# Kernel optimization log

Measured on AMD Instinct MI355X. Metric: run time of the kernel, lower is better.

The kernel has to match this reference:

```python
import jax, jax.numpy as jnp
import numpy as np

N = 262144      # number of points
K = 16          # KNN neighbors -> fixed degree CSR
E = N * K
CLASS_DIM = 40


def setup_inputs() -> dict:
    key = jax.random.key(0)
    ks = jax.random.split(key, 12)
    x = jax.random.normal(ks[0], (N, 3), dtype=jnp.float32)
    indptr = (jnp.arange(N + 1, dtype=jnp.int32) * K)
    indices = jax.random.randint(ks[1], (E,), 0, N, dtype=jnp.int32)

    def xavier(k, fan_out, fan_in):
        bound = np.sqrt(6.0 / (fan_in + fan_out)).astype(np.float32)
        return jax.random.uniform(k, (fan_out, fan_in), dtype=jnp.float32,
                                  minval=-bound, maxval=bound)

    return {
        "x": x, "indptr": indptr, "indices": indices,
        "w1": xavier(ks[2], 64, 3),
        "w2": xavier(ks[3], 64, 64),
        "w3": xavier(ks[4], 64, 64),
        "w4": xavier(ks[5], 128, 64),
        "w5": xavier(ks[6], 1024, 192),
        "wf1": xavier(ks[7], 512, 1024),
        "wf2": xavier(ks[8], 256, 512),
        "wf3": xavier(ks[9], CLASS_DIM, 256),
    }


def reference(x, indptr, indices, w1, w2, w3, w4, w5, wf1, wf2, wf3):
    # mlp1, mlp2 (bias-free Linear + ReLU)
    h = jax.nn.relu(x @ w1.T)          # [N, 64]
    h = jax.nn.relu(h @ w2.T)          # [N, 64]

    # GraphMaxPooling: CSR neighbor max (segment-max over gathered rows)
    n = h.shape[0]
    e = indices.shape[0]
    deg = indptr[1:] - indptr[:-1]                                   # [N]
    seg = jnp.repeat(jnp.arange(n, dtype=jnp.int32), deg,
                     total_repeat_length=e)                          # [E]
    x_gm = jax.ops.segment_max(h[indices], seg, num_segments=n,
                               indices_are_sorted=True)              # [N, 64]

    # mlp3, mlp4
    h3 = jax.nn.relu(h @ w3.T)         # [N, 64]
    h4 = jax.nn.relu(h3 @ w4.T)        # [N, 128]

    # concat neighbor-pooled features with point features, mlp5
    hc = jnp.concatenate([x_gm, h4], axis=1)   # [N, 192]
    h5 = jax.nn.relu(hc @ w5.T)                # [N, 1024]

    # global max pool over points -> [1, 1024]
    g = jnp.max(h5, axis=0, keepdims=True)

    # classifier head (dropout in eval mode = identity)
    f = jax.nn.relu(g @ wf1.T)
    f = jax.nn.relu(f @ wf2.T)
    return f @ wf3.T                            # [1, class_dim]
```

## Files before the change

kernel.cpp:

```cpp
#include <hip/hip_runtime.h>
#include <hip/hip_bf16.h>
#include <stdint.h>

typedef unsigned short u16;
typedef __bf16 bf16x8 __attribute__((ext_vector_type(8)));
typedef float  f32x4  __attribute__((ext_vector_type(4)));
typedef u16    u16x8  __attribute__((ext_vector_type(8)));

__device__ __forceinline__ float bf2f(u16 u) {
    return __uint_as_float(((unsigned)u) << 16);
}
__device__ __forceinline__ u16 f2bf(float f) {
    unsigned u = __float_as_uint(f);
    u += 0x7fffu + ((u >> 16) & 1u);
    return (u16)(u >> 16);
}
__device__ __forceinline__ u16x8 maxu16(u16x8 a, u16x8 b) {
    u16x8 r;
    #pragma unroll
    for (int e = 0; e < 8; ++e) r[e] = a[e] > b[e] ? a[e] : b[e];
    return r;
}
__device__ __forceinline__ u16x8 shfl_xor16(u16x8 v, int mask) {
    union { u16x8 u; int i[4]; } a, r;
    a.u = v;
    #pragma unroll
    for (int t = 0; t < 4; ++t) r.i[t] = __shfl_xor(a.i[t], mask, 64);
    return r.u;
}

#define MFMA16(a, b, c) __builtin_amdgcn_mfma_f32_16x16x32_bf16(a, b, c, 0, 0, 0)

__device__ u16   h2g_buf[262144 * 64];
__device__ u16   gm_buf [262144 * 64];
__device__ u16   w3b[64 * 64];
__device__ u16   w4b[128 * 64];
__device__ u16   w5b[1024 * 192];
__device__ float g_buf[1024];
__device__ float f1_buf[512];
__device__ float f2_buf[256];

__global__ void k0_zero() { g_buf[threadIdx.x] = 0.f; }

__global__ void kcvt(const float* __restrict__ w3f, const float* __restrict__ w4f,
                     const float* __restrict__ w5f)
{
    int i = blockIdx.x * 256 + threadIdx.x;
    if (i < 4096)        w3b[i]         = f2bf(w3f[i]);
    else if (i < 12288)  w4b[i - 4096]  = f2bf(w4f[i - 4096]);
    else                 w5b[i - 12288] = f2bf(w5f[i - 12288]);
}

__global__ __launch_bounds__(256) void k1_mlp(
    const float* __restrict__ xf, const float* __restrict__ w1f,
    const float* __restrict__ w2f)
{
    __shared__ __align__(16) u16 sw1[64 * 4];
    __shared__ __align__(16) u16 sx [64 * 4];
    __shared__ __align__(16) u16 sw2[64 * 72];
    __shared__ __align__(16) u16 shA[64 * 72];
    __shared__ __align__(16) u16 sh2[64 * 72];

    const int tid = threadIdx.x;
    const int p0  = blockIdx.x * 64;

    for (int i = tid; i < 64 * 64; i += 256)
        sw2[(i >> 6) * 72 + (i & 63)] = f2bf(w2f[i]);
    if (tid < 192) {
        sw1[(tid / 3) * 4 + tid % 3] = f2bf(w1f[tid]);
        sx [(tid / 3) * 4 + tid % 3] = f2bf(xf[p0 * 3 + tid]);
    }
    __syncthreads();

    {
        int m = tid & 63, ng = tid >> 6;
        float x0 = bf2f(sx[m * 4]), x1 = bf2f(sx[m * 4 + 1]), x2 = bf2f(sx[m * 4 + 2]);
        #pragma unroll
        for (int j = 0; j < 16; ++j) {
            int n = ng * 16 + j;
            float s = x0 * bf2f(sw1[n * 4]) + x1 * bf2f(sw1[n * 4 + 1]) + x2 * bf2f(sw1[n * 4 + 2]);
            shA[m * 72 + n] = f2bf(fmaxf(s, 0.f));
        }
    }
    __syncthreads();

    const int lane = tid & 63, w = tid >> 6, q = lane >> 4, l15 = lane & 15;
    const int mrow = 16 * w;

    f32x4 acc2[4];
    #pragma unroll
    for (int nt = 0; nt < 4; ++nt) acc2[nt] = (f32x4){0.f, 0.f, 0.f, 0.f};
    #pragma unroll
    for (int s = 0; s < 2; ++s) {
        bf16x8 a = *(const bf16x8*)&shA[(mrow + l15) * 72 + s * 32 + q * 8];
        #pragma unroll
        for (int nt = 0; nt < 4; ++nt) {
            bf16x8 b = *(const bf16x8*)&sw2[(nt * 16 + l15) * 72 + s * 32 + q * 8];
            acc2[nt] = MFMA16(a, b, acc2[nt]);
        }
    }
    #pragma unroll
    for (int nt = 0; nt < 4; ++nt)
        #pragma unroll
        for (int r = 0; r < 4; ++r) {
            int m = mrow + q * 4 + r;
            sh2[m * 72 + nt * 16 + l15] = f2bf(fmaxf(acc2[nt][r], 0.f));
        }
    __syncthreads();

    {
        int row = tid >> 2, c = (tid & 3) * 16;
        *(u16x8*)&h2g_buf[(size_t)p0 * 64 + tid * 16]     = *(const u16x8*)&sh2[row * 72 + c];
        *(u16x8*)&h2g_buf[(size_t)p0 * 64 + tid * 16 + 8] = *(const u16x8*)&sh2[row * 72 + c + 8];
    }
}

__global__ __launch_bounds__(256) void k2_pool(const int* __restrict__ idx)
{
    const size_t p = (blockIdx.x << 2) | (threadIdx.x >> 6);
    const int lane = threadIdx.x & 63;
    const int k = lane >> 3, c = lane & 7;

    int j0 = idx[p * 16 + k];
    int j1 = idx[p * 16 + 8 + k];
    u16x8 a = *(const u16x8*)&h2g_buf[(size_t)j0 * 64 + c * 8];
    u16x8 b = *(const u16x8*)&h2g_buf[(size_t)j1 * 64 + c * 8];
    u16x8 m = maxu16(a, b);
    m = maxu16(m, shfl_xor16(m, 8));
    m = maxu16(m, shfl_xor16(m, 16));
    m = maxu16(m, shfl_xor16(m, 32));
    if (lane < 8)
        *(u16x8*)&gm_buf[p * 64 + lane * 8] = m;
}

__global__ __launch_bounds__(256) void k3_fused(int* __restrict__ g)
{
    __shared__ __align__(16) u16 lds[128 * 192 + 2 * 128 * 64];
    u16* sA  = lds;
    u16* sB0 = lds + 24576;
    u16* sB1 = lds + 24576 + 8192;

    const int tid  = threadIdx.x;
    const size_t R0 = (size_t)blockIdx.x * 128;
    const int lane = tid & 63, w = tid >> 6, q = lane >> 4, l15 = lane & 15;
    const int m0w  = (w & 1) * 64, n0w = (w >> 1) * 64;

    #pragma unroll
    for (int c = 0; c < 4; ++c) {
        int i = c * 256 + tid, r = i >> 3, js = i & 7;
        *(u16x8*)&sB0[r * 64 + ((js ^ r) & 7) * 8] =
            *(const u16x8*)&h2g_buf[(R0 + r) * 64 + js * 8];
    }
    #pragma unroll
    for (int c = 0; c < 4; ++c) {
        int i = c * 256 + tid, r = i >> 3, js = i & 7;
        *(u16x8*)&sA[r * 192 + ((js ^ r) & 7) * 8] =
            *(const u16x8*)&gm_buf[(R0 + r) * 64 + js * 8];
    }
    __syncthreads();

    {
        f32x4 a3[2][4];
        #pragma unroll
        for (int mt = 0; mt < 2; ++mt)
            #pragma unroll
            for (int nt = 0; nt < 4; ++nt) a3[mt][nt] = (f32x4){0.f, 0.f, 0.f, 0.f};
        #pragma unroll
        for (int ss = 0; ss < 2; ++ss) {
            bf16x8 a[2], b[4];
            #pragma unroll
            for (int mt = 0; mt < 2; ++mt) {
                int r = w * 32 + mt * 16 + l15;
                a[mt] = *(const bf16x8*)&sB0[r * 64 + (((ss * 4 + q) ^ r) & 7) * 8];
            }
            #pragma unroll
            for (int nt = 0; nt < 4; ++nt)
                b[nt] = *(const bf16x8*)&w3b[(nt * 16 + l15) * 64 + ss * 32 + q * 8];
            #pragma unroll
            for (int mt = 0; mt < 2; ++mt)
                #pragma unroll
                for (int nt = 0; nt < 4; ++nt)
                    a3[mt][nt] = MFMA16(a[mt], b[nt], a3[mt][nt]);
        }
        __syncthreads();
        #pragma unroll
        for (int mt = 0; mt < 2; ++mt)
            #pragma unroll
            for (int nt = 0; nt < 4; ++nt)
                #pragma unroll
                for (int r = 0; r < 4; ++r) {
                    int m = w * 32 + mt * 16 + q * 4 + r;
                    int n = nt * 16 + l15;
                    sB0[m * 64 + (((n >> 3) ^ m) & 7) * 8 + (n & 7)] =
                        f2bf(fmaxf(a3[mt][nt][r], 0.f));
                }
    }
    __syncthreads();

    {
        f32x4 a4[2][8];
        #pragma unroll
        for (int mt = 0; mt < 2; ++mt)
            #pragma unroll
            for (int nt = 0; nt < 8; ++nt) a4[mt][nt] = (f32x4){0.f, 0.f, 0.f, 0.f};
        #pragma unroll
        for (int ss = 0; ss < 2; ++ss) {
            bf16x8 a[2];
            #pragma unroll
            for (int mt = 0; mt < 2; ++mt) {
                int r = w * 32 + mt * 16 + l15;
                a[mt] = *(const bf16x8*)&sB0[r * 64 + (((ss * 4 + q) ^ r) & 7) * 8];
            }
            #pragma unroll
            for (int nt = 0; nt < 8; ++nt) {
                bf16x8 b = *(const bf16x8*)&w4b[(nt * 16 + l15) * 64 + ss * 32 + q * 8];
                #pragma unroll
                for (int mt = 0; mt < 2; ++mt)
                    a4[mt][nt] = MFMA16(a[mt], b, a4[mt][nt]);
            }
        }
        #pragma unroll
        for (int mt = 0; mt < 2; ++mt)
            #pragma unroll
            for (int nt = 0; nt < 8; ++nt)
                #pragma unroll
                for (int r = 0; r < 4; ++r) {
                    int m  = w * 32 + mt * 16 + q * 4 + r;
                    int n4 = nt * 16 + l15;
                    int j  = 8 + (n4 >> 3);
                    int p  = (j & 24) | ((j ^ m) & 7);
                    sA[m * 192 + p * 8 + (n4 & 7)] = f2bf(fmaxf(a4[mt][nt][r], 0.f));
                }
    }
    __syncthreads();

    u16x8 v[4];
    #pragma unroll
    for (int c = 0; c < 4; ++c) {
        int i = c * 256 + tid, r = i >> 3, js = i & 7;
        v[c] = *(const u16x8*)&w5b[(size_t)r * 192 + js * 8];
    }
    #pragma unroll
    for (int c = 0; c < 4; ++c) {
        int i = c * 256 + tid, r = i >> 3, js = i & 7;
        *(u16x8*)&sB0[r * 64 + ((js ^ r) & 7) * 8] = v[c];
    }

    int s = 0;
    for (int bn = 0; bn < 8; ++bn) {
        f32x4 acc[4][4];
        #pragma unroll
        for (int mt = 0; mt < 4; ++mt)
            #pragma unroll
            for (int nt = 0; nt < 4; ++nt) acc[mt][nt] = (f32x4){0.f, 0.f, 0.f, 0.f};

        for (int kt = 0; kt < 3; ++kt, ++s) {
            if (s < 23) {
                int s1 = s + 1, bn1 = s1 / 3, kt1 = s1 - bn1 * 3;
                #pragma unroll
                for (int c = 0; c < 4; ++c) {
                    int i = c * 256 + tid, r = i >> 3, js = i & 7;
                    v[c] = *(const u16x8*)&w5b[(size_t)(bn1 * 128 + r) * 192 + kt1 * 64 + js * 8];
                }
            }
            __syncthreads();
            const u16* sBc = (s & 1) ? sB1 : sB0;
            #pragma unroll
            for (int ss = 0; ss < 2; ++ss) {
                bf16x8 a[4], b[4];
                #pragma unroll
                for (int mt = 0; mt < 4; ++mt) {
                    int r = m0w + mt * 16 + l15;
                    int p = (kt * 8) | (((ss * 4 + q) ^ r) & 7);
                    a[mt] = *(const bf16x8*)&sA[r * 192 + p * 8];
                }
                #pragma unroll
                for (int nt = 0; nt < 4; ++nt) {
                    int r = n0w + nt * 16 + l15;
                    b[nt] = *(const bf16x8*)&sBc[r * 64 + (((ss * 4 + q) ^ r) & 7) * 8];
                }
                #pragma unroll
                for (int mt = 0; mt < 4; ++mt)
                    #pragma unroll
                    for (int nt = 0; nt < 4; ++nt)
                        acc[mt][nt] = MFMA16(a[mt], b[nt], acc[mt][nt]);
            }
            if (s < 23) {
                u16* sBn = (s & 1) ? sB0 : sB1;
                #pragma unroll
                for (int c = 0; c < 4; ++c) {
                    int i = c * 256 + tid, r = i >> 3, js = i & 7;
                    *(u16x8*)&sBn[r * 64 + ((js ^ r) & 7) * 8] = v[c];
                }
            }
        }

        #pragma unroll
        for (int nt = 0; nt < 4; ++nt) {
            float mx = 0.f;
            #pragma unroll
            for (int mt = 0; mt < 4; ++mt)
                #pragma unroll
                for (int r = 0; r < 4; ++r) mx = fmaxf(mx, acc[mt][nt][r]);
            mx = fmaxf(mx, __shfl_xor(mx, 16, 64));
            mx = fmaxf(mx, __shfl_xor(mx, 32, 64));
            if (q == 0) {
                int col = bn * 128 + n0w + nt * 16 + l15;
                atomicMax(&g[col], __float_as_int(mx));
            }
        }
    }
}

__global__ void k4_f1(const float* __restrict__ wf1)
{
    int r = blockIdx.x, l = threadIdx.x;
    float s = 0.f;
    #pragma unroll
    for (int i = 0; i < 16; ++i) s += wf1[r * 1024 + i * 64 + l] * g_buf[i * 64 + l];
    #pragma unroll
    for (int o = 32; o; o >>= 1) s += __shfl_down(s, o, 64);
    if (!l) f1_buf[r] = fmaxf(s, 0.f);
}
__global__ void k4_f2(const float* __restrict__ wf2)
{
    int r = blockIdx.x, l = threadIdx.x;
    float s = 0.f;
    #pragma unroll
    for (int i = 0; i < 8; ++i) s += wf2[r * 512 + i * 64 + l] * f1_buf[i * 64 + l];
    #pragma unroll
    for (int o = 32; o; o >>= 1) s += __shfl_down(s, o, 64);
    if (!l) f2_buf[r] = fmaxf(s, 0.f);
}
__global__ void k4_out(const float* __restrict__ wf3, float* __restrict__ out)
{
    int r = blockIdx.x, l = threadIdx.x;
    float s = 0.f;
    #pragma unroll
    for (int i = 0; i < 4; ++i) s += wf3[r * 256 + i * 64 + l] * f2_buf[i * 64 + l];
    #pragma unroll
    for (int o = 32; o; o >>= 1) s += __shfl_down(s, o, 64);
    if (!l) out[r] = s;
}

extern "C" void kernel_launch(void* const* d_in, const int* in_sizes, int n_in,
                              void* d_out, int out_size, void* d_ws, size_t ws_size,
                              hipStream_t stream)
{
    (void)in_sizes; (void)n_in; (void)out_size; (void)d_ws; (void)ws_size;
    const float* x   = (const float*)d_in[0];
    const int*   idx = (const int*)d_in[2];
    const float* w1  = (const float*)d_in[3];
    const float* w2  = (const float*)d_in[4];
    const float* w3  = (const float*)d_in[5];
    const float* w4  = (const float*)d_in[6];
    const float* w5  = (const float*)d_in[7];
    const float* wf1 = (const float*)d_in[8];
    const float* wf2 = (const float*)d_in[9];
    const float* wf3 = (const float*)d_in[10];

    float* gptr;
    hipGetSymbolAddress((void**)&gptr, HIP_SYMBOL(g_buf));

    k0_zero <<<1, 1024, 0, stream>>>();
    kcvt    <<<816, 256, 0, stream>>>(w3, w4, w5);
    k1_mlp  <<<262144 / 64, 256, 0, stream>>>(x, w1, w2);
    k2_pool <<<262144 / 4, 256, 0, stream>>>(idx);
    k3_fused<<<262144 / 128, 256, 0, stream>>>((int*)gptr);
    k4_f1   <<<512, 64, 0, stream>>>(wf1);
    k4_f2   <<<256, 64, 0, stream>>>(wf2);
    k4_out  <<<40, 64, 0, stream>>>(wf3, (float*)d_out);
}
```

Baseline: 476.5 us.

## Keep mlp5 operands in registers, drop LDS B staging, batch pool gathers

The pooling kernel now has each wave handle four points, so each lane issues eight independent row gathers before reducing, which should improve memory-level parallelism and cut the block count. The fused kernel removes the double-buffered LDS staging of w5 and instead streams w5 fragments from global/L2 straight into registers, prefetching one k-step ahead. It also preloads all A fragments for mlp5 into registers and packs the h2/h3 tiles into spare columns of the sA buffer, which removes several __syncthreads. LDS use shrinks, which could raise occupancy, but register pressure grows sharply (about 96 VGPRs for areg plus the B buffers and accumulators) and the uncoalesced per-lane global loads of w5 could hurt.

```diff
diff --git a/kernel.cpp b/kernel.cpp
--- a/kernel.cpp
+++ b/kernel.cpp
@@ -117,28 +117,40 @@
 
 __global__ __launch_bounds__(256) void k2_pool(const int* __restrict__ idx)
 {
-    const size_t p = (blockIdx.x << 2) | (threadIdx.x >> 6);
+    const int wv   = threadIdx.x >> 6;
+    const size_t p0 = ((size_t)blockIdx.x * 4 + wv) * 4;
     const int lane = threadIdx.x & 63;
     const int k = lane >> 3, c = lane & 7;
 
-    int j0 = idx[p * 16 + k];
-    int j1 = idx[p * 16 + 8 + k];
-    u16x8 a = *(const u16x8*)&h2g_buf[(size_t)j0 * 64 + c * 8];
-    u16x8 b = *(const u16x8*)&h2g_buf[(size_t)j1 * 64 + c * 8];
-    u16x8 m = maxu16(a, b);
-    m = maxu16(m, shfl_xor16(m, 8));
-    m = maxu16(m, shfl_xor16(m, 16));
-    m = maxu16(m, shfl_xor16(m, 32));
-    if (lane < 8)
-        *(u16x8*)&gm_buf[p * 64 + lane * 8] = m;
+    int js[8];
+    #pragma unroll
+    for (int t = 0; t < 4; ++t) {
+        js[2 * t]     = idx[(p0 + t) * 16 + k];
+        js[2 * t + 1] = idx[(p0 + t) * 16 + 8 + k];
+    }
+    u16x8 v[8];
+    #pragma unroll
+    for (int u = 0; u < 8; ++u)
+        v[u] = *(const u16x8*)&h2g_buf[(size_t)js[u] * 64 + c * 8];
+
+    u16x8 m[4];
+    #pragma unroll
+    for (int t = 0; t < 4; ++t) {
+        u16x8 mm = maxu16(v[2 * t], v[2 * t + 1]);
+        mm = maxu16(mm, shfl_xor16(mm, 8));
+        mm = maxu16(mm, shfl_xor16(mm, 16));
+        mm = maxu16(mm, shfl_xor16(mm, 32));
+        m[t] = mm;
+    }
+    if (lane < 32) {
+        u16x8 out = (k == 0) ? m[0] : (k == 1) ? m[1] : (k == 2) ? m[2] : m[3];
+        *(u16x8*)&gm_buf[(p0 + k) * 64 + c * 8] = out;
+    }
 }
 
 __global__ __launch_bounds__(256) void k3_fused(int* __restrict__ g)
 {
-    __shared__ __align__(16) u16 lds[128 * 192 + 2 * 128 * 64];
-    u16* sA  = lds;
-    u16* sB0 = lds + 24576;
-    u16* sB1 = lds + 24576 + 8192;
+    __shared__ __align__(16) u16 sA[128 * 192];
 
     const int tid  = threadIdx.x;
     const size_t R0 = (size_t)blockIdx.x * 128;
@@ -148,14 +160,10 @@
     #pragma unroll
     for (int c = 0; c < 4; ++c) {
         int i = c * 256 + tid, r = i >> 3, js = i & 7;
-        *(u16x8*)&sB0[r * 64 + ((js ^ r) & 7) * 8] =
-            *(const u16x8*)&h2g_buf[(R0 + r) * 64 + js * 8];
-    }
-    #pragma unroll
-    for (int c = 0; c < 4; ++c) {
-        int i = c * 256 + tid, r = i >> 3, js = i & 7;
         *(u16x8*)&sA[r * 192 + ((js ^ r) & 7) * 8] =
             *(const u16x8*)&gm_buf[(R0 + r) * 64 + js * 8];
+        *(u16x8*)&sA[r * 192 + (8 | ((js ^ r) & 7)) * 8] =
+            *(const u16x8*)&h2g_buf[(R0 + r) * 64 + js * 8];
     }
     __syncthreads();
 
@@ -167,11 +175,12 @@
             for (int nt = 0; nt < 4; ++nt) a3[mt][nt] = (f32x4){0.f, 0.f, 0.f, 0.f};
         #pragma unroll
         for (int ss = 0; ss < 2; ++ss) {
+            int js = ss * 4 + q;
             bf16x8 a[2], b[4];
             #pragma unroll
             for (int mt = 0; mt < 2; ++mt) {
                 int r = w * 32 + mt * 16 + l15;
-                a[mt] = *(const bf16x8*)&sB0[r * 64 + (((ss * 4 + q) ^ r) & 7) * 8];
+                a[mt] = *(const bf16x8*)&sA[r * 192 + (8 | ((js ^ r) & 7)) * 8];
             }
             #pragma unroll
             for (int nt = 0; nt < 4; ++nt)
@@ -182,7 +191,6 @@
                 for (int nt = 0; nt < 4; ++nt)
                     a3[mt][nt] = MFMA16(a[mt], b[nt], a3[mt][nt]);
         }
-        __syncthreads();
         #pragma unroll
         for (int mt = 0; mt < 2; ++mt)
             #pragma unroll
@@ -191,11 +199,10 @@
                 for (int r = 0; r < 4; ++r) {
                     int m = w * 32 + mt * 16 + q * 4 + r;
                     int n = nt * 16 + l15;
-                    sB0[m * 64 + (((n >> 3) ^ m) & 7) * 8 + (n & 7)] =
+                    sA[m * 192 + (16 | (((n >> 3) ^ m) & 7)) * 8 + (n & 7)] =
                         f2bf(fmaxf(a3[mt][nt][r], 0.f));
                 }
     }
-    __syncthreads();
 
     {
         f32x4 a4[2][8];
@@ -205,11 +212,12 @@
             for (int nt = 0; nt < 8; ++nt) a4[mt][nt] = (f32x4){0.f, 0.f, 0.f, 0.f};
         #pragma unroll
         for (int ss = 0; ss < 2; ++ss) {
+            int js = ss * 4 + q;
             bf16x8 a[2];
             #pragma unroll
             for (int mt = 0; mt < 2; ++mt) {
                 int r = w * 32 + mt * 16 + l15;
-                a[mt] = *(const bf16x8*)&sB0[r * 64 + (((ss * 4 + q) ^ r) & 7) * 8];
+                a[mt] = *(const bf16x8*)&sA[r * 192 + (16 | ((js ^ r) & 7)) * 8];
             }
             #pragma unroll
             for (int nt = 0; nt < 8; ++nt) {
@@ -234,19 +242,29 @@
     }
     __syncthreads();
 
-    u16x8 v[4];
-    #pragma unroll
-    for (int c = 0; c < 4; ++c) {
-        int i = c * 256 + tid, r = i >> 3, js = i & 7;
-        v[c] = *(const u16x8*)&w5b[(size_t)r * 192 + js * 8];
-    }
-    #pragma unroll
-    for (int c = 0; c < 4; ++c) {
-        int i = c * 256 + tid, r = i >> 3, js = i & 7;
-        *(u16x8*)&sB0[r * 64 + ((js ^ r) & 7) * 8] = v[c];
-    }
-
-    int s = 0;
+    bf16x8 areg[3][2][4];
+    #pragma unroll
+    for (int kt = 0; kt < 3; ++kt)
+        #pragma unroll
+        for (int ss = 0; ss < 2; ++ss) {
+            int js = ss * 4 + q;
+            #pragma unroll
+            for (int mt = 0; mt < 4; ++mt) {
+                int r = m0w + mt * 16 + l15;
+                int p = (kt * 8) | ((js ^ r) & 7);
+                areg[kt][ss][mt] = *(const bf16x8*)&sA[r * 192 + p * 8];
+            }
+        }
+
+    const size_t bbase = (size_t)(n0w + l15) * 192 + q * 8;
+    bf16x8 bc[2][4], bx[2][4];
+    #pragma unroll
+    for (int ss = 0; ss < 2; ++ss)
+        #pragma unroll
+        for (int nt = 0; nt < 4; ++nt)
+            bc[ss][nt] = *(const bf16x8*)&w5b[bbase + (size_t)nt * 3072 + ss * 32];
+
+    int bn1 = 0, kt1 = 1;
     for (int bn = 0; bn < 8; ++bn) {
         f32x4 acc[4][4];
         #pragma unroll
@@ -254,45 +272,28 @@
             #pragma unroll
             for (int nt = 0; nt < 4; ++nt) acc[mt][nt] = (f32x4){0.f, 0.f, 0.f, 0.f};
 
-        for (int kt = 0; kt < 3; ++kt, ++s) {
-            if (s < 23) {
-                int s1 = s + 1, bn1 = s1 / 3, kt1 = s1 - bn1 * 3;
-                #pragma unroll
-                for (int c = 0; c < 4; ++c) {
-                    int i = c * 256 + tid, r = i >> 3, js = i & 7;
-                    v[c] = *(const u16x8*)&w5b[(size_t)(bn1 * 128 + r) * 192 + kt1 * 64 + js * 8];
-                }
-            }
-            __syncthreads();
-            const u16* sBc = (s & 1) ? sB1 : sB0;
-            #pragma unroll
-            for (int ss = 0; ss < 2; ++ss) {
-                bf16x8 a[4], b[4];
-                #pragma unroll
-                for (int mt = 0; mt < 4; ++mt) {
-                    int r = m0w + mt * 16 + l15;
-                    int p = (kt * 8) | (((ss * 4 + q) ^ r) & 7);
-                    a[mt] = *(const bf16x8*)&sA[r * 192 + p * 8];
-                }
-                #pragma unroll
-                for (int nt = 0; nt < 4; ++nt) {
-                    int r = n0w + nt * 16 + l15;
-                    b[nt] = *(const bf16x8*)&sBc[r * 64 + (((ss * 4 + q) ^ r) & 7) * 8];
-                }
+        #pragma unroll
+        for (int kt = 0; kt < 3; ++kt) {
+            if (bn * 3 + kt < 23) {
+                size_t nb = bbase + (size_t)bn1 * 24576 + kt1 * 64;
+                #pragma unroll
+                for (int ss = 0; ss < 2; ++ss)
+                    #pragma unroll
+                    for (int nt = 0; nt < 4; ++nt)
+                        bx[ss][nt] = *(const bf16x8*)&w5b[nb + (size_t)nt * 3072 + ss * 32];
+                if (++kt1 == 3) { kt1 = 0; ++bn1; }
+            }
+            #pragma unroll
+            for (int ss = 0; ss < 2; ++ss)
                 #pragma unroll
                 for (int mt = 0; mt < 4; ++mt)
                     #pragma unroll
                     for (int nt = 0; nt < 4; ++nt)
-                        acc[mt][nt] = MFMA16(a[mt], b[nt], acc[mt][nt]);
-            }
-            if (s < 23) {
-                u16* sBn = (s & 1) ? sB0 : sB1;
-                #pragma unroll
-                for (int c = 0; c < 4; ++c) {
-                    int i = c * 256 + tid, r = i >> 3, js = i & 7;
-                    *(u16x8*)&sBn[r * 64 + ((js ^ r) & 7) * 8] = v[c];
-                }
-            }
+                        acc[mt][nt] = MFMA16(areg[kt][ss][mt], bc[ss][nt], acc[mt][nt]);
+            #pragma unroll
+            for (int ss = 0; ss < 2; ++ss)
+                #pragma unroll
+                for (int nt = 0; nt < 4; ++nt) bc[ss][nt] = bx[ss][nt];
         }
 
         #pragma unroll
@@ -365,7 +366,7 @@
     k0_zero <<<1, 1024, 0, stream>>>();
     kcvt    <<<816, 256, 0, stream>>>(w3, w4, w5);
     k1_mlp  <<<262144 / 64, 256, 0, stream>>>(x, w1, w2);
-    k2_pool <<<262144 / 4, 256, 0, stream>>>(idx);
+    k2_pool <<<262144 / 16, 256, 0, stream>>>(idx);
     k3_fused<<<262144 / 128, 256, 0, stream>>>((int*)gptr);
     k4_f1   <<<512, 64, 0, stream>>>(wf1);
     k4_f2   <<<256, 64, 0, stream>>>(wf2);
```

New measurement: 581.8 us. +22.1%, slower.

## Rework neighbor pooling per thread and keep mlp5 A operands in registers

Applied to the files above, without the earlier changes.

The pooling kernel now gives each thread one 8-channel slice of one point and loops over all 16 neighbors, so the cross-lane shuffle reductions go away. In the fused kernel, h2 and h3 are staged in spare columns of the sA tile instead of reusing sB0, which removes two block barriers. The mlp5 A fragments are loaded from LDS once into registers and reused across all 8 N-blocks instead of being reloaded every k-step. The trade is much higher register pressure (96 VGPRs of A fragments plus a 64-register accumulator), which may cut occupancy or cause spills.

```diff
diff --git a/kernel.cpp b/kernel.cpp
--- a/kernel.cpp
+++ b/kernel.cpp
@@ -20,13 +20,6 @@
     #pragma unroll
     for (int e = 0; e < 8; ++e) r[e] = a[e] > b[e] ? a[e] : b[e];
     return r;
-}
-__device__ __forceinline__ u16x8 shfl_xor16(u16x8 v, int mask) {
-    union { u16x8 u; int i[4]; } a, r;
-    a.u = v;
-    #pragma unroll
-    for (int t = 0; t < 4; ++t) r.i[t] = __shfl_xor(a.i[t], mask, 64);
-    return r.u;
 }
 
 #define MFMA16(a, b, c) __builtin_amdgcn_mfma_f32_16x16x32_bf16(a, b, c, 0, 0, 0)
@@ -117,20 +110,20 @@
 
 __global__ __launch_bounds__(256) void k2_pool(const int* __restrict__ idx)
 {
-    const size_t p = (blockIdx.x << 2) | (threadIdx.x >> 6);
-    const int lane = threadIdx.x & 63;
-    const int k = lane >> 3, c = lane & 7;
-
-    int j0 = idx[p * 16 + k];
-    int j1 = idx[p * 16 + 8 + k];
-    u16x8 a = *(const u16x8*)&h2g_buf[(size_t)j0 * 64 + c * 8];
-    u16x8 b = *(const u16x8*)&h2g_buf[(size_t)j1 * 64 + c * 8];
-    u16x8 m = maxu16(a, b);
-    m = maxu16(m, shfl_xor16(m, 8));
-    m = maxu16(m, shfl_xor16(m, 16));
-    m = maxu16(m, shfl_xor16(m, 32));
-    if (lane < 8)
-        *(u16x8*)&gm_buf[p * 64 + lane * 8] = m;
+    const size_t gt = (size_t)blockIdx.x * 256 + threadIdx.x;
+    const size_t p  = gt >> 3;
+    const int    c  = (threadIdx.x & 7) * 8;
+
+    u16x8 v[16];
+    #pragma unroll
+    for (int k = 0; k < 16; ++k) {
+        int j = idx[p * 16 + k];
+        v[k] = *(const u16x8*)&h2g_buf[(size_t)j * 64 + c];
+    }
+    u16x8 m = v[0];
+    #pragma unroll
+    for (int k = 1; k < 16; ++k) m = maxu16(m, v[k]);
+    *(u16x8*)&gm_buf[p * 64 + c] = m;
 }
 
 __global__ __launch_bounds__(256) void k3_fused(int* __restrict__ g)
@@ -148,14 +141,10 @@
     #pragma unroll
     for (int c = 0; c < 4; ++c) {
         int i = c * 256 + tid, r = i >> 3, js = i & 7;
-        *(u16x8*)&sB0[r * 64 + ((js ^ r) & 7) * 8] =
-            *(const u16x8*)&h2g_buf[(R0 + r) * 64 + js * 8];
-    }
-    #pragma unroll
-    for (int c = 0; c < 4; ++c) {
-        int i = c * 256 + tid, r = i >> 3, js = i & 7;
         *(u16x8*)&sA[r * 192 + ((js ^ r) & 7) * 8] =
             *(const u16x8*)&gm_buf[(R0 + r) * 64 + js * 8];
+        *(u16x8*)&sA[r * 192 + (8 | ((js ^ r) & 7)) * 8] =
+            *(const u16x8*)&h2g_buf[(R0 + r) * 64 + js * 8];
     }
     __syncthreads();
 
@@ -167,11 +156,12 @@
             for (int nt = 0; nt < 4; ++nt) a3[mt][nt] = (f32x4){0.f, 0.f, 0.f, 0.f};
         #pragma unroll
         for (int ss = 0; ss < 2; ++ss) {
+            int js = ss * 4 + q;
             bf16x8 a[2], b[4];
             #pragma unroll
             for (int mt = 0; mt < 2; ++mt) {
                 int r = w * 32 + mt * 16 + l15;
-                a[mt] = *(const bf16x8*)&sB0[r * 64 + (((ss * 4 + q) ^ r) & 7) * 8];
+                a[mt] = *(const bf16x8*)&sA[r * 192 + (8 | ((js ^ r) & 7)) * 8];
             }
             #pragma unroll
             for (int nt = 0; nt < 4; ++nt)
@@ -182,7 +172,6 @@
                 for (int nt = 0; nt < 4; ++nt)
                     a3[mt][nt] = MFMA16(a[mt], b[nt], a3[mt][nt]);
         }
-        __syncthreads();
         #pragma unroll
         for (int mt = 0; mt < 2; ++mt)
             #pragma unroll
@@ -191,11 +180,10 @@
                 for (int r = 0; r < 4; ++r) {
                     int m = w * 32 + mt * 16 + q * 4 + r;
                     int n = nt * 16 + l15;
-                    sB0[m * 64 + (((n >> 3) ^ m) & 7) * 8 + (n & 7)] =
+                    sA[m * 192 + (16 | (((n >> 3) ^ m) & 7)) * 8 + (n & 7)] =
                         f2bf(fmaxf(a3[mt][nt][r], 0.f));
                 }
     }
-    __syncthreads();
 
     {
         f32x4 a4[2][8];
@@ -205,11 +193,12 @@
             for (int nt = 0; nt < 8; ++nt) a4[mt][nt] = (f32x4){0.f, 0.f, 0.f, 0.f};
         #pragma unroll
         for (int ss = 0; ss < 2; ++ss) {
+            int js = ss * 4 + q;
             bf16x8 a[2];
             #pragma unroll
             for (int mt = 0; mt < 2; ++mt) {
                 int r = w * 32 + mt * 16 + l15;
-                a[mt] = *(const bf16x8*)&sB0[r * 64 + (((ss * 4 + q) ^ r) & 7) * 8];
+                a[mt] = *(const bf16x8*)&sA[r * 192 + (16 | ((js ^ r) & 7)) * 8];
             }
             #pragma unroll
             for (int nt = 0; nt < 8; ++nt) {
@@ -234,6 +223,20 @@
     }
     __syncthreads();
 
+    bf16x8 areg[3][2][4];
+    #pragma unroll
+    for (int kt = 0; kt < 3; ++kt)
+        #pragma unroll
+        for (int ss = 0; ss < 2; ++ss) {
+            int js = ss * 4 + q;
+            #pragma unroll
+            for (int mt = 0; mt < 4; ++mt) {
+                int r = m0w + mt * 16 + l15;
+                int p = (kt * 8) | ((js ^ r) & 7);
+                areg[kt][ss][mt] = *(const bf16x8*)&sA[r * 192 + p * 8];
+            }
+        }
+
     u16x8 v[4];
     #pragma unroll
     for (int c = 0; c < 4; ++c) {
@@ -254,6 +257,7 @@
             #pragma unroll
             for (int nt = 0; nt < 4; ++nt) acc[mt][nt] = (f32x4){0.f, 0.f, 0.f, 0.f};
 
+        #pragma unroll
         for (int kt = 0; kt < 3; ++kt, ++s) {
             if (s < 23) {
                 int s1 = s + 1, bn1 = s1 / 3, kt1 = s1 - bn1 * 3;
@@ -265,26 +269,23 @@
             }
             __syncthreads();
             const u16* sBc = (s & 1) ? sB1 : sB0;
+            bf16x8 b[2][4];
             #pragma unroll
             for (int ss = 0; ss < 2; ++ss) {
-                bf16x8 a[4], b[4];
-                #pragma unroll
-                for (int mt = 0; mt < 4; ++mt) {
-                    int r = m0w + mt * 16 + l15;
-                    int p = (kt * 8) | (((ss * 4 + q) ^ r) & 7);
-                    a[mt] = *(const bf16x8*)&sA[r * 192 + p * 8];
-                }
+                int js = ss * 4 + q;
                 #pragma unroll
                 for (int nt = 0; nt < 4; ++nt) {
                     int r = n0w + nt * 16 + l15;
-                    b[nt] = *(const bf16x8*)&sBc[r * 64 + (((ss * 4 + q) ^ r) & 7) * 8];
-                }
+                    b[ss][nt] = *(const bf16x8*)&sBc[r * 64 + ((js ^ r) & 7) * 8];
+                }
+            }
+            #pragma unroll
+            for (int ss = 0; ss < 2; ++ss)
                 #pragma unroll
                 for (int mt = 0; mt < 4; ++mt)
                     #pragma unroll
                     for (int nt = 0; nt < 4; ++nt)
-                        acc[mt][nt] = MFMA16(a[mt], b[nt], acc[mt][nt]);
-            }
+                        acc[mt][nt] = MFMA16(areg[kt][ss][mt], b[ss][nt], acc[mt][nt]);
             if (s < 23) {
                 u16* sBn = (s & 1) ? sB0 : sB1;
                 #pragma unroll
@@ -365,7 +366,7 @@
     k0_zero <<<1, 1024, 0, stream>>>();
     kcvt    <<<816, 256, 0, stream>>>(w3, w4, w5);
     k1_mlp  <<<262144 / 64, 256, 0, stream>>>(x, w1, w2);
-    k2_pool <<<262144 / 4, 256, 0, stream>>>(idx);
+    k2_pool <<<262144 * 8 / 256, 256, 0, stream>>>(idx);
     k3_fused<<<262144 / 128, 256, 0, stream>>>((int*)gptr);
     k4_f1   <<<512, 64, 0, stream>>>(wf1);
     k4_f2   <<<256, 64, 0, stream>>>(wf2);
```

After: 459.2 us. 3.6% less time.
